# Kernel optimization log

Measured on AMD Instinct MI355X. Metric: run time of the kernel, lower is better.

Reference implementation:

```python
import jax, jax.numpy as jnp
import numpy as np

D_MODEL = 1024
NUM_HEADS = 16
HEAD_DIM = D_MODEL // NUM_HEADS
SCALE = HEAD_DIM ** -0.5


def setup_inputs() -> dict:
    key = jax.random.key(0)
    ks = jax.random.split(key, 5)
    x = jax.random.normal(ks[0], (2, 2048, D_MODEL), dtype=jnp.float32)
    w_qkv = jax.random.normal(ks[1], (D_MODEL, 3 * D_MODEL), dtype=jnp.float32) * (D_MODEL ** -0.5)
    b_qkv = jnp.zeros((3 * D_MODEL,), dtype=jnp.float32)
    w_out = jax.random.normal(ks[2], (D_MODEL, D_MODEL), dtype=jnp.float32) * (D_MODEL ** -0.5)
    b_out = jnp.zeros((D_MODEL,), dtype=jnp.float32)
    return {"x": x, "w_qkv": w_qkv, "b_qkv": b_qkv, "w_out": w_out, "b_out": b_out}


def reference(x, w_qkv, b_qkv, w_out, b_out):
    b, t, _ = x.shape
    qkv = x @ w_qkv + b_qkv  # [b, t, 3*d_model]
    q, k, v = jnp.split(qkv, 3, axis=-1)
    # b t (h d) -> b h t d
    def heads(z):
        return z.reshape(b, t, NUM_HEADS, HEAD_DIM).transpose(0, 2, 1, 3)
    q, k, v = heads(q), heads(k), heads(v)
    scores = jnp.einsum('bhtd,bhsd->bhts', q, k) * SCALE
    causal = jnp.tril(jnp.ones((t, t), dtype=bool))  # True = keep
    scores = jnp.where(causal, scores, -jnp.inf)
    weights = jax.nn.softmax(scores, axis=-1)
    out = jnp.einsum('bhts,bhsd->bhtd', weights, v)
    out = out.transpose(0, 2, 1, 3).reshape(b, t, D_MODEL)  # b h t d -> b t (h d)
    return out @ w_out + b_out
```

## Files before the change

kernel.cpp:

```cpp
#include <hip/hip_runtime.h>

#define D_MODEL 1024
#define NHEADS 16
#define HDIM 64
#define SEQ 2048
#define BATCH 2
#define M_TOTAL (BATCH * SEQ)
#define N_QKV (3 * D_MODEL)

typedef __attribute__((ext_vector_type(8))) short short8;
typedef __attribute__((ext_vector_type(4))) float f32x4;
typedef __attribute__((ext_vector_type(4))) unsigned short u16x4;
typedef unsigned short u16;

__device__ __forceinline__ u16 f2bf(float f) {
  union { float f; unsigned u; } v; v.f = f;
  unsigned u = v.u + 0x7fffu + ((v.u >> 16) & 1u);
  return (u16)(u >> 16);
}

__device__ __forceinline__ void gload_lds16(const void* g, void* l) {
  __builtin_amdgcn_global_load_lds(
      (__attribute__((address_space(1))) void*)(g),
      (__attribute__((address_space(3))) void*)(l),
      16, 0, 0);
}

__global__ void k_cvt_bf16(const float* __restrict__ src, u16* __restrict__ dst, int n4) {
  int i = blockIdx.x * blockDim.x + threadIdx.x;
  if (i >= n4) return;
  const float4 v = reinterpret_cast<const float4*>(src)[i];
  u16x4 o;
  o.x = f2bf(v.x); o.y = f2bf(v.y); o.z = f2bf(v.z); o.w = f2bf(v.w);
  reinterpret_cast<u16x4*>(dst)[i] = o;
}

__global__ void k_transpose_bf16(const float* __restrict__ src, u16* __restrict__ dst, int R, int C) {
  __shared__ float tile[32][33];
  const int bx = blockIdx.x * 32;
  const int by = blockIdx.y * 32;
  const int tx = threadIdx.x, ty = threadIdx.y;
  #pragma unroll
  for (int i = ty; i < 32; i += 8) tile[i][tx] = src[(size_t)(by + i) * C + bx + tx];
  __syncthreads();
  #pragma unroll
  for (int i = ty; i < 32; i += 8) dst[(size_t)(bx + i) * R + by + tx] = f2bf(tile[tx][i]);
}

template <int K, int BM, int BN, int WC>
__device__ __forceinline__ void gemm_core(const u16* __restrict__ A, const u16* __restrict__ Bt,
                                          int m0, int n0, u16* As, u16* Bs, f32x4* acc) {
  constexpr int WR = 4 / WC;
  constexpr int MI = BM / WR / 16;
  constexpr int NI = BN / WC / 16;
  const int tid = threadIdx.x;
  const int lane = tid & 63;
  const int lr = lane & 15, lg = lane >> 4;
  const int wid = tid >> 6;
  const int wr = (wid / WC) * (BM / WR);
  const int wc = (wid % WC) * (BN / WC);
  for (int kt = 0; kt < K; kt += 32) {
    #pragma unroll
    for (int r = 0; r < BM / 64; ++r) {
      const int off = r * 4096 + tid * 16;
      const int row = off >> 6, colb = off & 63;
      gload_lds16((const char*)A + ((size_t)(m0 + row) * K + kt) * 2 + colb, (char*)As + off);
    }
    #pragma unroll
    for (int r = 0; r < BN / 64; ++r) {
      const int off = r * 4096 + tid * 16;
      const int row = off >> 6, colb = off & 63;
      gload_lds16((const char*)Bt + ((size_t)(n0 + row) * K + kt) * 2 + colb, (char*)Bs + off);
    }
    __syncthreads();
    short8 a[MI], b[NI];
    #pragma unroll
    for (int i = 0; i < MI; ++i) a[i] = *(const short8*)&As[(wr + i * 16 + lr) * 32 + lg * 8];
    #pragma unroll
    for (int i = 0; i < NI; ++i) b[i] = *(const short8*)&Bs[(wc + i * 16 + lr) * 32 + lg * 8];
    #pragma unroll
    for (int mi = 0; mi < MI; ++mi)
      #pragma unroll
      for (int ni = 0; ni < NI; ++ni)
        acc[mi * NI + ni] = __builtin_amdgcn_mfma_f32_16x16x32_bf16(a[mi], b[ni], acc[mi * NI + ni], 0, 0, 0);
    __syncthreads();
  }
}

__global__ __launch_bounds__(256) void k_gemm_qkv(const u16* __restrict__ A, const u16* __restrict__ Bt,
                                                  const float* __restrict__ bias,
                                                  u16* __restrict__ qb, u16* __restrict__ kb,
                                                  u16* __restrict__ vb) {
  __shared__ u16 As[128 * 32];
  __shared__ u16 Bs[128 * 32];
  f32x4 acc[16] = {};
  const int m0 = blockIdx.x * 128, n0 = blockIdx.y * 128;
  gemm_core<D_MODEL, 128, 128, 2>(A, Bt, m0, n0, As, Bs, acc);
  const int lane = threadIdx.x & 63, lr = lane & 15, lg = lane >> 4;
  const int wid = threadIdx.x >> 6;
  const int wr = (wid >> 1) * 64, wc = (wid & 1) * 64;
  #pragma unroll
  for (int ni = 0; ni < 4; ++ni) {
    const int col = n0 + wc + ni * 16 + lr;
    const float bv = bias[col];
    const int which = col >> 10;
    const int h = (col >> 6) & 15;
    const int d = col & 63;
    #pragma unroll
    for (int mi = 0; mi < 4; ++mi) {
      #pragma unroll
      for (int j = 0; j < 4; ++j) {
        const int rw = m0 + wr + mi * 16 + lg * 4 + j;
        const int bb = rw >> 11, t = rw & (SEQ - 1);
        const u16 val = f2bf(acc[mi * 4 + ni][j] + bv);
        const int bh = bb * NHEADS + h;
        if (which == 0)      qb[((size_t)bh * SEQ + t) * HDIM + d] = val;
        else if (which == 1) kb[((size_t)bh * SEQ + t) * HDIM + d] = val;
        else                 vb[((size_t)bh * HDIM + d) * SEQ + t] = val;
      }
    }
  }
}

__global__ __launch_bounds__(256) void k_gemm_out(const u16* __restrict__ A, const u16* __restrict__ Bt,
                                                  const float* __restrict__ bias,
                                                  float* __restrict__ out) {
  __shared__ u16 As[64 * 32];
  __shared__ u16 Bs[128 * 32];
  f32x4 acc[8] = {};
  const int m0 = blockIdx.x * 64, n0 = blockIdx.y * 128;
  gemm_core<D_MODEL, 64, 128, 4>(A, Bt, m0, n0, As, Bs, acc);
  const int lane = threadIdx.x & 63, lr = lane & 15, lg = lane >> 4;
  const int wid = threadIdx.x >> 6;
  const int wc = wid * 32;
  #pragma unroll
  for (int ni = 0; ni < 2; ++ni) {
    const int col = n0 + wc + ni * 16 + lr;
    const float bv = bias[col];
    #pragma unroll
    for (int mi = 0; mi < 4; ++mi) {
      #pragma unroll
      for (int j = 0; j < 4; ++j) {
        const int rw = m0 + mi * 16 + lg * 4 + j;
        out[(size_t)rw * D_MODEL + col] = acc[mi * 2 + ni][j] + bv;
      }
    }
  }
}

__global__ __launch_bounds__(512) void k_attn(const u16* __restrict__ qb, const u16* __restrict__ kb,
                                              const u16* __restrict__ vb, u16* __restrict__ attn) {
  __shared__ u16 Ks[2][64 * 64];
  __shared__ u16 Vs[2][64 * 64];
  __shared__ u16 Pl[8][16 * 64];
  const int tid = threadIdx.x, lane = tid & 63, wid = tid >> 6;
  const int lr = lane & 15, lg = lane >> 4;
  const int bh = blockIdx.y, b = bh >> 4, h = bh & 15;
  const int q0 = ((int)gridDim.x - 1 - (int)blockIdx.x) * 128;
  const int qw = q0 + wid * 16;
  const u16* Q = qb + (size_t)bh * SEQ * HDIM;
  const u16* Kp = kb + (size_t)bh * SEQ * HDIM;
  const u16* Vp = vb + (size_t)bh * HDIM * SEQ;
  u16* Pw = &Pl[wid][0];

  auto stage = [&](int buf, int st_) {
    const int s0_ = st_ * 64;
    const int off = tid * 16;
    const int row = off >> 7;
    const int colb = (off & 127) ^ ((row & 7) << 4);
    gload_lds16((const char*)Kp + (size_t)(s0_ + row) * (HDIM * 2) + colb, (char*)&Ks[buf][0] + off);
    gload_lds16((const char*)Vp + ((size_t)row * SEQ + s0_) * 2 + colb, (char*)&Vs[buf][0] + off);
  };

  short8 aq[2];
  #pragma unroll
  for (int ks = 0; ks < 2; ++ks)
    aq[ks] = *(const short8*)&Q[(size_t)(qw + lr) * HDIM + ks * 32 + lg * 8];

  short8 onesf;
  #pragma unroll
  for (int e = 0; e < 8; ++e) onesf[e] = (short)0x3F80;

  f32x4 acc[4] = {};
  f32x4 accl = {};

  const float sc = 0.125f * 1.44269504089f;
  const float FM = 12.0f;
  const int ntile = q0 / 64 + 2;

  stage(0, 0);
  __syncthreads();

  for (int st = 0; st < ntile; ++st) {
    const int s0 = st * 64;
    const int cur = st & 1;
    if (st + 1 < ntile) stage(cur ^ 1, st + 1);

    if (s0 <= qw + 15) {
      const char* Kt = (const char*)&Ks[cur][0];
      const char* Vt = (const char*)&Vs[cur][0];

      f32x4 s[4] = {};
      #pragma unroll
      for (int ks = 0; ks < 2; ++ks) {
        #pragma unroll
        for (int ni = 0; ni < 4; ++ni) {
          const int row = ni * 16 + lr;
          const short8 kf = *(const short8*)(Kt + row * 128 + ((ks * 64 + lg * 16) ^ ((row & 7) << 4)));
          s[ni] = __builtin_amdgcn_mfma_f32_16x16x32_bf16(aq[ks], kf, s[ni], 0, 0, 0);
        }
      }

      const bool need_mask = (s0 + 63 > qw);
      #pragma unroll
      for (int ni = 0; ni < 4; ++ni)
        #pragma unroll
        for (int j = 0; j < 4; ++j) {
          float v = s[ni][j] * sc - FM;
          if (need_mask) {
            const int qq = qw + lg * 4 + j;
            const int ss = s0 + ni * 16 + lr;
            v = (ss > qq) ? -1e30f : v;
          }
          s[ni][j] = exp2f(v);
        }

      #pragma unroll
      for (int ni = 0; ni < 4; ++ni)
        #pragma unroll
        for (int j = 0; j < 4; ++j) {
          const int row = lg * 4 + j;
          const int col = ni * 16 + lr;
          const int byte = (row * 128 + col * 2) ^ ((row & 7) << 4);
          *(u16*)((char*)Pw + byte) = f2bf(s[ni][j]);
        }

      #pragma unroll
      for (int ks = 0; ks < 2; ++ks) {
        const int byte = (lr * 128 + ks * 64 + lg * 16) ^ ((lr & 7) << 4);
        const short8 pa = *(const short8*)((const char*)Pw + byte);
        accl = __builtin_amdgcn_mfma_f32_16x16x32_bf16(pa, onesf, accl, 0, 0, 0);
        #pragma unroll
        for (int ni = 0; ni < 4; ++ni) {
          const int row = ni * 16 + lr;
          const short8 vfr = *(const short8*)(Vt + row * 128 + ((ks * 64 + lg * 16) ^ ((row & 7) << 4)));
          acc[ni] = __builtin_amdgcn_mfma_f32_16x16x32_bf16(pa, vfr, acc[ni], 0, 0, 0);
        }
      }
    }

    __syncthreads();
  }

  #pragma unroll
  for (int j = 0; j < 4; ++j) {
    const float inv = 1.f / accl[j];
    const int t = qw + lg * 4 + j;
    #pragma unroll
    for (int ni = 0; ni < 4; ++ni) {
      const int col = h * HDIM + ni * 16 + lr;
      attn[((size_t)b * SEQ + t) * D_MODEL + col] = f2bf(acc[ni][j] * inv);
    }
  }
}

extern "C" void kernel_launch(void* const* d_in, const int* in_sizes, int n_in,
                              void* d_out, int out_size, void* d_ws, size_t ws_size,
                              hipStream_t stream) {
  const float* x     = (const float*)d_in[0];
  const float* w_qkv = (const float*)d_in[1];
  const float* b_qkv = (const float*)d_in[2];
  const float* w_out = (const float*)d_in[3];
  const float* b_out = (const float*)d_in[4];
  float* out = (float*)d_out;

  char* ws = (char*)d_ws;
  u16* xb    = (u16*)(ws);
  u16* wqkvT = (u16*)(ws + ((size_t)8 << 20));
  u16* woutT = (u16*)(ws + ((size_t)14 << 20));
  u16* qbuf  = (u16*)(ws + ((size_t)16 << 20));
  u16* kbuf  = (u16*)(ws + ((size_t)24 << 20));
  u16* vbuf  = (u16*)(ws + ((size_t)32 << 20));
  u16* attn  = (u16*)(ws + ((size_t)40 << 20));

  k_cvt_bf16<<<(M_TOTAL * D_MODEL / 4 + 255) / 256, 256, 0, stream>>>(x, xb, M_TOTAL * D_MODEL / 4);
  k_transpose_bf16<<<dim3(N_QKV / 32, D_MODEL / 32), dim3(32, 8), 0, stream>>>(w_qkv, wqkvT, D_MODEL, N_QKV);
  k_transpose_bf16<<<dim3(D_MODEL / 32, D_MODEL / 32), dim3(32, 8), 0, stream>>>(w_out, woutT, D_MODEL, D_MODEL);
  k_gemm_qkv<<<dim3(M_TOTAL / 128, N_QKV / 128), 256, 0, stream>>>(xb, wqkvT, b_qkv, qbuf, kbuf, vbuf);
  k_attn<<<dim3(SEQ / 128, BATCH * NHEADS), 512, 0, stream>>>(qbuf, kbuf, vbuf, attn);
  k_gemm_out<<<dim3(M_TOTAL / 64, D_MODEL / 128), 256, 0, stream>>>(attn, woutT, b_out, out);
}
```

Before: 219.0 us.

## Shrink attention blocks to 64 queries with balanced causal scheduling and packed P stores

The attention kernel now uses 256-thread blocks covering 64 query rows, launched as a 1D grid of 1024 blocks. Block indices are remapped so causal query tiles alternate between long and short rows across heads, which is meant to balance per-block work and cut the tail. The MFMA operands are swapped so the score layout lets each lane write packed 8-byte bf16 runs into LDS instead of scalar 2-byte stores. In exchange, each block re-loads K/V tiles for fewer queries, raising total K/V traffic.

Result: faster. 199.5 us (-8.9%).

```diff
diff --git a/kernel.cpp b/kernel.cpp
--- a/kernel.cpp
+++ b/kernel.cpp
@@ -17,6 +17,10 @@
   union { float f; unsigned u; } v; v.f = f;
   unsigned u = v.u + 0x7fffu + ((v.u >> 16) & 1u);
   return (u16)(u >> 16);
+}
+
+__device__ __forceinline__ unsigned pack_bf16(float lo, float hi) {
+  return (unsigned)f2bf(lo) | ((unsigned)f2bf(hi) << 16);
 }
 
 __device__ __forceinline__ void gload_lds16(const void* g, void* l) {
@@ -148,15 +152,20 @@
   }
 }
 
-__global__ __launch_bounds__(512) void k_attn(const u16* __restrict__ qb, const u16* __restrict__ kb,
+__global__ __launch_bounds__(256) void k_attn(const u16* __restrict__ qb, const u16* __restrict__ kb,
                                               const u16* __restrict__ vb, u16* __restrict__ attn) {
   __shared__ u16 Ks[2][64 * 64];
   __shared__ u16 Vs[2][64 * 64];
-  __shared__ u16 Pl[8][16 * 64];
+  __shared__ u16 Pl[4][16 * 64];
   const int tid = threadIdx.x, lane = tid & 63, wid = tid >> 6;
   const int lr = lane & 15, lg = lane >> 4;
-  const int bh = blockIdx.y, b = bh >> 4, h = bh & 15;
-  const int q0 = ((int)gridDim.x - 1 - (int)blockIdx.x) * 128;
+  const int lin = blockIdx.x;
+  const int r = lin >> 8, c = lin & 255;
+  const int a = c >> 3;
+  const int qrank = (r & 1) ? a : (31 - a);
+  const int bh = (c & 7) | (r << 3);
+  const int b = bh >> 4, h = bh & 15;
+  const int q0 = qrank * 64;
   const int qw = q0 + wid * 16;
   const u16* Q = qb + (size_t)bh * SEQ * HDIM;
   const u16* Kp = kb + (size_t)bh * SEQ * HDIM;
@@ -165,11 +174,14 @@
 
   auto stage = [&](int buf, int st_) {
     const int s0_ = st_ * 64;
-    const int off = tid * 16;
-    const int row = off >> 7;
-    const int colb = (off & 127) ^ ((row & 7) << 4);
-    gload_lds16((const char*)Kp + (size_t)(s0_ + row) * (HDIM * 2) + colb, (char*)&Ks[buf][0] + off);
-    gload_lds16((const char*)Vp + ((size_t)row * SEQ + s0_) * 2 + colb, (char*)&Vs[buf][0] + off);
+    #pragma unroll
+    for (int rr = 0; rr < 2; ++rr) {
+      const int off = rr * 4096 + tid * 16;
+      const int row = off >> 7;
+      const int colb = (off & 127) ^ ((row & 7) << 4);
+      gload_lds16((const char*)Kp + (size_t)(s0_ + row) * (HDIM * 2) + colb, (char*)&Ks[buf][0] + off);
+      gload_lds16((const char*)Vp + ((size_t)row * SEQ + s0_) * 2 + colb, (char*)&Vs[buf][0] + off);
+    }
   };
 
   short8 aq[2];
@@ -186,7 +198,7 @@
 
   const float sc = 0.125f * 1.44269504089f;
   const float FM = 12.0f;
-  const int ntile = q0 / 64 + 2;
+  const int ntile = qrank + 1;
 
   stage(0, 0);
   __syncthreads();
@@ -207,33 +219,32 @@
         for (int ni = 0; ni < 4; ++ni) {
           const int row = ni * 16 + lr;
           const short8 kf = *(const short8*)(Kt + row * 128 + ((ks * 64 + lg * 16) ^ ((row & 7) << 4)));
-          s[ni] = __builtin_amdgcn_mfma_f32_16x16x32_bf16(aq[ks], kf, s[ni], 0, 0, 0);
+          s[ni] = __builtin_amdgcn_mfma_f32_16x16x32_bf16(kf, aq[ks], s[ni], 0, 0, 0);
         }
       }
 
       const bool need_mask = (s0 + 63 > qw);
+      const int qq = qw + lr;
       #pragma unroll
       for (int ni = 0; ni < 4; ++ni)
         #pragma unroll
         for (int j = 0; j < 4; ++j) {
           float v = s[ni][j] * sc - FM;
           if (need_mask) {
-            const int qq = qw + lg * 4 + j;
-            const int ss = s0 + ni * 16 + lr;
+            const int ss = s0 + ni * 16 + lg * 4 + j;
             v = (ss > qq) ? -1e30f : v;
           }
           s[ni][j] = exp2f(v);
         }
 
       #pragma unroll
-      for (int ni = 0; ni < 4; ++ni)
-        #pragma unroll
-        for (int j = 0; j < 4; ++j) {
-          const int row = lg * 4 + j;
-          const int col = ni * 16 + lr;
-          const int byte = (row * 128 + col * 2) ^ ((row & 7) << 4);
-          *(u16*)((char*)Pw + byte) = f2bf(s[ni][j]);
-        }
+      for (int ni = 0; ni < 4; ++ni) {
+        uint2 w;
+        w.x = pack_bf16(s[ni][0], s[ni][1]);
+        w.y = pack_bf16(s[ni][2], s[ni][3]);
+        const int byte = (lr * 128 + ni * 32 + lg * 8) ^ ((lr & 7) << 4);
+        *(uint2*)((char*)Pw + byte) = w;
+      }
 
       #pragma unroll
       for (int ks = 0; ks < 2; ++ks) {
@@ -287,6 +298,6 @@
   k_transpose_bf16<<<dim3(N_QKV / 32, D_MODEL / 32), dim3(32, 8), 0, stream>>>(w_qkv, wqkvT, D_MODEL, N_QKV);
   k_transpose_bf16<<<dim3(D_MODEL / 32, D_MODEL / 32), dim3(32, 8), 0, stream>>>(w_out, woutT, D_MODEL, D_MODEL);
   k_gemm_qkv<<<dim3(M_TOTAL / 128, N_QKV / 128), 256, 0, stream>>>(xb, wqkvT, b_qkv, qbuf, kbuf, vbuf);
-  k_attn<<<dim3(SEQ / 128, BATCH * NHEADS), 512, 0, stream>>>(qbuf, kbuf, vbuf, attn);
+  k_attn<<<1024, 256, 0, stream>>>(qbuf, kbuf, vbuf, attn);
   k_gemm_out<<<dim3(M_TOTAL / 64, D_MODEL / 128), 256, 0, stream>>>(attn, woutT, b_out, out);
 }
```
